# Performance work log

Hardware: AMD Instinct MI355X
Metric: run time of the kernel (lower is better)

Reference implementation:

```python
import jax, jax.numpy as jnp
import numpy as np

# model dims
B, T, D, H, FF, L, V = 2, 1024, 1024, 16, 4096, 2, 32000
DH = D // H          # head dim 64
M = 32               # num attention blocks
BS = T // M          # block size 32
TOPK = 8             # quality-selected blocks per batch element
RATIO = 0.25         # low-pass ratio for spectral quality score
THETA = 10000.0      # rope base
EPS = 1e-6


def setup_inputs() -> dict:
    key = jax.random.key(0)
    ks = jax.random.split(key, 12)
    s = 0.02
    f32 = jnp.float32
    return {
        "input_ids": jax.random.randint(ks[0], (B, T), 0, V),
        "emb": jax.random.normal(ks[1], (V, D), f32) * s,
        "wq": jax.random.normal(ks[2], (L, D, D), f32) * s,
        "wk": jax.random.normal(ks[3], (L, D, D), f32) * s,
        "wv": jax.random.normal(ks[4], (L, D, D), f32) * s,
        "wo": jax.random.normal(ks[5], (L, D, D), f32) * s,
        "w1": jax.random.normal(ks[6], (L, D, FF), f32) * s,
        "w2": jax.random.normal(ks[7], (L, FF, D), f32) * s,
        "w3": jax.random.normal(ks[8], (L, D, FF), f32) * s,
        "attn_norm": jnp.ones((L, D), f32),
        "ffn_norm": jnp.ones((L, D), f32),
        "final_norm": jnp.ones((D,), f32),
        "lm_head": jax.random.normal(ks[9], (D, V), f32) * s,
    }


def _rms(x, w):
    return x * jax.lax.rsqrt(jnp.mean(x * x, axis=-1, keepdims=True) + EPS) * w


def _rope_tables():
    inv = 1.0 / (THETA ** (jnp.arange(0, DH, 2, dtype=jnp.float32) / DH))
    pos = jnp.arange(T, dtype=jnp.float32)
    freqs = pos[:, None] * inv[None, :]            # [T, DH/2]
    emb = jnp.concatenate([freqs, freqs], axis=-1)  # [T, DH]
    return jnp.cos(emb)[None, None], jnp.sin(emb)[None, None]  # [1,1,T,DH]


def _rotate_half(x):
    h = x.shape[-1] // 2
    return jnp.concatenate([-x[..., h:], x[..., :h]], axis=-1)


def _quality_score(h):
    # spectral quality rho(t): low-frequency energy ratio along the sequence axis
    Hf = jnp.fft.rfft(h, axis=1)                   # [B, T//2+1, D] complex
    nf = Hf.shape[1]
    keep = max(1, int(nf * RATIO))
    lp_mask = (jnp.arange(nf) < keep)[None, :, None]
    h_lp = jnp.fft.irfft(jnp.where(lp_mask, Hf, 0.0), n=T, axis=1)
    return jnp.sum(h_lp * h_lp, axis=-1) / (jnp.sum(h * h, axis=-1) + EPS)  # [B,T]


def _forward(input_ids, emb, wq, wk, wv, wo, w1, w2, w3,
             attn_norm, ffn_norm, final_norm, lm_head):
    x = emb[input_ids]                             # [B,T,D]

    # per-token quality (computed once, cached across layers) -> block quality
    rho = _quality_score(x)                        # [B,T]
    blk_quality = rho.reshape(B, M, BS).mean(axis=-1)  # [B,M]

    # quality routing: select top-k blocks per batch element
    _, sel_idx = jax.lax.top_k(blk_quality, TOPK)  # [B,TOPK]
    selected = jnp.zeros((B, M), dtype=bool).at[jnp.arange(B)[:, None], sel_idx].set(True)

    # block-sparse causal mask: causal AND (kv block selected OR same block as query)
    blk_id = jnp.arange(T) // BS                   # [T]
    causal = jnp.tril(jnp.ones((T, T), dtype=bool))
    same_block = blk_id[:, None] == blk_id[None, :]
    allowed_kv = selected[:, blk_id]               # [B,T]
    mask = causal[None] & (allowed_kv[:, None, :] | same_block[None])  # [B,T,T]
    bias = jnp.where(mask, 0.0, -1e9)[:, None]     # [B,1,T,T]

    cos, sin = _rope_tables()
    scale = 1.0 / np.sqrt(DH)

    for l in range(L):
        # attention
        h = _rms(x, attn_norm[l])
        q = (h @ wq[l]).reshape(B, T, H, DH).transpose(0, 2, 1, 3)
        k = (h @ wk[l]).reshape(B, T, H, DH).transpose(0, 2, 1, 3)
        v = (h @ wv[l]).reshape(B, T, H, DH).transpose(0, 2, 1, 3)
        q = q * cos + _rotate_half(q) * sin
        k = k * cos + _rotate_half(k) * sin
        scores = jnp.einsum('bhqd,bhkd->bhqk', q, k) * scale + bias
        attn = jax.nn.softmax(scores, axis=-1)
        o = jnp.einsum('bhqk,bhkd->bhqd', attn, v).transpose(0, 2, 1, 3).reshape(B, T, D)
        x = x + o @ wo[l]
        # swiglu feed-forward
        h = _rms(x, ffn_norm[l])
        x = x + (jax.nn.silu(h @ w1[l]) * (h @ w3[l])) @ w2[l]

    x = _rms(x, final_norm)
    return x @ lm_head                             # [B,T,V]


def reference(input_ids, emb, wq, wk, wv, wo, w1, w2, w3,
              attn_norm, ffn_norm, final_norm, lm_head):
    return _forward(input_ids, emb, wq, wk, wv, wo, w1, w2, w3,
                    attn_norm, ffn_norm, final_norm, lm_head)
```

## Files before the change

kernel.cpp:

```cpp
#include <hip/hip_runtime.h>
#include <hip/hip_bf16.h>

#define Bn 2
#define Tn 1024
#define Dn 1024
#define Hn 16
#define DHn 64
#define FFn 4096
#define Ln 2
#define Vn 32000
#define GM 2048

typedef unsigned short u16;
typedef __attribute__((ext_vector_type(4))) float f4;
typedef __attribute__((ext_vector_type(4))) unsigned short us4;
typedef __attribute__((ext_vector_type(8))) unsigned short us8;
typedef __attribute__((ext_vector_type(8))) short short8;
typedef __attribute__((ext_vector_type(4))) float f32x4;

__device__ __forceinline__ u16 f2b(float x) {
  union { __hip_bfloat16 h; u16 u; } v; v.h = __float2bfloat16(x); return v.u;
}
__device__ __forceinline__ float b2f(u16 u) {
  union { unsigned int i; float f; } v; v.i = ((unsigned int)u) << 16; return v.f;
}
__device__ __forceinline__ float wred64(float v) {
#pragma unroll
  for (int m = 32; m > 0; m >>= 1) v += __shfl_xor(v, m);
  return v;
}
__device__ __forceinline__ void gload_lds16(const void* g, void* l) {
  __builtin_amdgcn_global_load_lds(
      (const __attribute__((address_space(1))) unsigned int*)g,
      (__attribute__((address_space(3))) unsigned int*)l, 16, 0, 0);
}

__global__ void rope_tab_kernel(float* COS, float* SIN) {
  int t = blockIdx.x;
  int j = threadIdx.x;
  float inv = __expf(-(float)(j & 31) * (9.210340371976184f / 32.f));
  float th = (float)t * inv;
  COS[t * 64 + j] = cosf(th);
  SIN[t * 64 + j] = sinf(th);
}

__global__ __launch_bounds__(256) void embed_kernel(const int* ids, const float* emb, float* x) {
  int g = blockIdx.x;
  int id = ids[g];
  const f4* src = (const f4*)(emb + (size_t)id * Dn);
  f4* dst = (f4*)(x + (size_t)g * Dn);
  dst[threadIdx.x] = src[threadIdx.x];
}

__global__ __launch_bounds__(256) void qa_kernel(const float* x, float* Ac, float* Bc) {
  __shared__ float ct[1024], st[1024];
  int blk = blockIdx.x;
  int b = blk >> 7, f = blk & 127;
  for (int t = threadIdx.x; t < 1024; t += 256) {
    float u = (float)((f * t) & 1023) * (6.283185307179586f / 1024.f);
    ct[t] = cosf(u); st[t] = sinf(u);
  }
  __syncthreads();
  int d0 = threadIdx.x * 4;
  f4 a = {0.f,0.f,0.f,0.f}, bb = {0.f,0.f,0.f,0.f};
  const float* xb = x + (size_t)b * Tn * Dn + d0;
  for (int t = 0; t < 1024; ++t) {
    f4 xv = *(const f4*)(xb + (size_t)t * Dn);
    float c = ct[t], s = st[t];
    a += xv * c; bb += xv * s;
  }
  size_t o = ((size_t)b * 128 + f) * Dn + d0;
  *(f4*)(Ac + o) = a; *(f4*)(Bc + o) = bb;
}

__global__ __launch_bounds__(256) void qr_kernel(const float* Ac, const float* Bc,
                                                 const float* x, float* rho) {
  __shared__ float phc[128][4], phs[128][4];
  __shared__ float redN[4], redD[4];
  int blk = blockIdx.x;
  int b = blk >> 8, t0 = (blk & 255) * 4;
  int tid = threadIdx.x;
#pragma unroll
  for (int rep = 0; rep < 2; ++rep) {
    int e = rep * 256 + tid;
    int f = e >> 2, tt = e & 3;
    float u = (float)((f * (t0 + tt)) & 1023) * (6.283185307179586f / 1024.f);
    phc[f][tt] = cosf(u); phs[f][tt] = sinf(u);
  }
  int d0 = tid * 4;
  const float* Ab = Ac + (size_t)b * 128 * Dn + d0;
  const float* Bb = Bc + (size_t)b * 128 * Dn + d0;
  f4 a0 = *(const f4*)Ab;
  float sacc[4][4];
#pragma unroll
  for (int tt = 0; tt < 4; ++tt)
#pragma unroll
    for (int c = 0; c < 4; ++c) sacc[tt][c] = 0.5f * a0[c];
  __syncthreads();
  for (int f = 1; f < 128; ++f) {
    f4 a = *(const f4*)(Ab + (size_t)f * Dn);
    f4 bb = *(const f4*)(Bb + (size_t)f * Dn);
#pragma unroll
    for (int tt = 0; tt < 4; ++tt) {
      float c = phc[f][tt], s = phs[f][tt];
#pragma unroll
      for (int e = 0; e < 4; ++e) sacc[tt][e] += a[e] * c + bb[e] * s;
    }
  }
  int wave = tid >> 6, lane = tid & 63;
  for (int tt = 0; tt < 4; ++tt) {
    f4 xv = *(const f4*)(x + ((size_t)b * Tn + t0 + tt) * Dn + d0);
    float num = 0.f, den = 0.f;
#pragma unroll
    for (int e = 0; e < 4; ++e) {
      float hl = sacc[tt][e] * (2.f / 1024.f);
      num += hl * hl;
      den += xv[e] * xv[e];
    }
    float rn = wred64(num), rd = wred64(den);
    if (lane == 0) { redN[wave] = rn; redD[wave] = rd; }
    __syncthreads();
    if (tid == 0) {
      float n = redN[0] + redN[1] + redN[2] + redN[3];
      float dd = redD[0] + redD[1] + redD[2] + redD[3];
      rho[(size_t)b * Tn + t0 + tt] = n / (dd + 1e-6f);
    }
    __syncthreads();
  }
}

__global__ void topk_kernel(const float* rho, int* sel) {
  __shared__ float bq[32];
  __shared__ int chosen[32];
  int b = blockIdx.x;
  int m = threadIdx.x;
  float s = 0.f;
  for (int j = 0; j < 32; ++j) s += rho[(size_t)b * Tn + m * 32 + j];
  bq[m] = s * (1.f / 32.f); chosen[m] = 0;
  __syncthreads();
  if (m == 0) {
    for (int it = 0; it < 8; ++it) {
      float best = -3e38f; int bi = 0;
      for (int mm = 0; mm < 32; ++mm) if (bq[mm] > best) { best = bq[mm]; bi = mm; }
      chosen[bi] = 1; bq[bi] = -3e38f;
    }
  }
  __syncthreads();
  sel[b * 32 + m] = chosen[m];
}

__global__ __launch_bounds__(256) void transpose_to_bf16(const float* src, u16* dst, int K, int N) {
  __shared__ float tile[32][33];
  int n0 = blockIdx.x * 32, k0 = blockIdx.y * 32;
  int c = threadIdx.x & 31, r4 = threadIdx.x >> 5;
#pragma unroll
  for (int rr = 0; rr < 4; ++rr) {
    int r = r4 * 4 + rr;
    tile[r][c] = src[(size_t)(k0 + r) * N + n0 + c];
  }
  __syncthreads();
#pragma unroll
  for (int rr = 0; rr < 4; ++rr) {
    int r = r4 * 4 + rr;
    dst[(size_t)(n0 + r) * K + k0 + c] = f2b(tile[c][r]);
  }
}

__global__ __launch_bounds__(256) void rmsnorm_kernel(const float* x, const float* w, u16* out) {
  __shared__ float red[4];
  int g = blockIdx.x;
  int tid = threadIdx.x;
  f4 xv = ((const f4*)(x + (size_t)g * Dn))[tid];
  float ss = xv[0]*xv[0] + xv[1]*xv[1] + xv[2]*xv[2] + xv[3]*xv[3];
  ss = wred64(ss);
  if ((tid & 63) == 0) red[tid >> 6] = ss;
  __syncthreads();
  float tot = red[0] + red[1] + red[2] + red[3];
  float r = rsqrtf(tot * (1.f / 1024.f) + 1e-6f);
  f4 wv = ((const f4*)w)[tid];
  us4 o;
#pragma unroll
  for (int e = 0; e < 4; ++e) o[e] = f2b(xv[e] * r * wv[e]);
  *(us4*)(out + (size_t)g * Dn + tid * 4) = o;
}

__global__ __launch_bounds__(256) void gemm_bf16_kernel(
    const u16* __restrict__ A, const u16* __restrict__ Bt,
    void* C, const float* R, int Ni, int Ki, int obf) {
  __shared__ short8 As[1024];
  __shared__ short8 Bs[1024];
  const int tid = threadIdx.x;
  const int wave = tid >> 6, lane = tid & 63;
  const int wr = wave >> 1, wc = wave & 1;
  const int lrow = lane & 15, lkg = lane >> 4;
  const size_t arow0 = (size_t)blockIdx.y * 128;
  const size_t bcol0 = (size_t)blockIdx.x * 128;
  const f32x4 zero4 = {0.f, 0.f, 0.f, 0.f};
  f32x4 acc[4][4];
#pragma unroll
  for (int i = 0; i < 4; ++i)
#pragma unroll
    for (int j = 0; j < 4; ++j) acc[i][j] = zero4;
  const int nK = Ki >> 6;
  for (int kb = 0; kb < nK; ++kb) {
    const size_t k0 = (size_t)kb << 6;
#pragma unroll
    for (int j = 0; j < 4; ++j) {
      const int p = j * 256 + tid;
      const int r = p >> 3, c = p & 7;
      const int cs = c ^ (r & 7);
      gload_lds16(A + (arow0 + r) * Ki + k0 + cs * 8, (char*)As + p * 16);
      gload_lds16(Bt + (bcol0 + r) * Ki + k0 + cs * 8, (char*)Bs + p * 16);
    }
    __syncthreads();
#pragma unroll
    for (int kk = 0; kk < 2; ++kk) {
      short8 af[4], bfr[4];
#pragma unroll
      for (int i = 0; i < 4; ++i) {
        const int ar = wr * 64 + i * 16 + lrow;
        const int akg = kk * 4 + lkg;
        af[i] = *(const short8*)((const char*)As + ar * 128 + ((akg ^ (ar & 7)) << 4));
        const int br = wc * 64 + i * 16 + lrow;
        bfr[i] = *(const short8*)((const char*)Bs + br * 128 + ((akg ^ (br & 7)) << 4));
      }
#pragma unroll
      for (int i = 0; i < 4; ++i)
#pragma unroll
        for (int j = 0; j < 4; ++j)
          acc[i][j] = __builtin_amdgcn_mfma_f32_16x16x32_bf16(af[i], bfr[j], acc[i][j], 0, 0, 0);
    }
    __syncthreads();
  }
  const int crow = (lane >> 4) * 4;
  const int ccol = lane & 15;
#pragma unroll
  for (int i = 0; i < 4; ++i)
#pragma unroll
    for (int j = 0; j < 4; ++j)
#pragma unroll
      for (int rg = 0; rg < 4; ++rg) {
        const size_t grow = arow0 + wr * 64 + i * 16 + crow + rg;
        const size_t gcol = bcol0 + wc * 64 + j * 16 + ccol;
        float v = acc[i][j][rg];
        if (obf) {
          ((u16*)C)[grow * Ni + gcol] = f2b(v);
        } else {
          if (R) v += R[grow * Ni + gcol];
          ((float*)C)[grow * Ni + gcol] = v;
        }
      }
}

__global__ __launch_bounds__(256) void rope_apply_kernel(const float* QKV, const float* COS, const float* SIN,
                                                         float* QRo, float* KRo, float* VRo) {
  int g = blockIdx.x;
  int b = g >> 10, t = g & 1023;
  int j = threadIdx.x * 4;
  int h = j >> 6, jd = j & 63;
  const float* base = QKV + (size_t)g * 3072;
  f4 q = *(const f4*)(base + j);
  f4 k = *(const f4*)(base + 1024 + j);
  f4 v = *(const f4*)(base + 2048 + j);
  int pj = (jd < 32) ? j + 32 : j - 32;
  f4 qp = *(const f4*)(base + pj);
  f4 kp = *(const f4*)(base + 1024 + pj);
  float sgn = (jd < 32) ? -1.f : 1.f;
  f4 cv = *(const f4*)(COS + t * 64 + jd);
  f4 sv = *(const f4*)(SIN + t * 64 + jd);
  f4 qr = q * cv + (qp * sgn) * sv;
  f4 kr = k * cv + (kp * sgn) * sv;
  size_t o = ((size_t)(b * Hn + h) * Tn + t) * 64 + jd;
  *(f4*)(QRo + o) = qr; *(f4*)(KRo + o) = kr; *(f4*)(VRo + o) = v;
}

__global__ __launch_bounds__(256) void attn_kernel(
    const float* __restrict__ QR, const float* __restrict__ KR, const float* __restrict__ VR,
    const int* __restrict__ sel, u16* __restrict__ O) {
  __shared__ float Qs[32][64], Ks[32][64], Vs[32][64], S[32][32];
  const int blk = blockIdx.x;
  const int mq = blk & 31, h = (blk >> 5) & 15, b = blk >> 9;
  const int tid = threadIdx.x;
  const size_t bh = (size_t)(b * Hn + h) * Tn;
  {
    const f4* q4 = (const f4*)(QR + (bh + mq * 32) * 64);
    f4* s4 = (f4*)&Qs[0][0];
    s4[tid] = q4[tid]; s4[tid + 256] = q4[tid + 256];
  }
  const int row = tid >> 3, dg = tid & 7;
  const int dh0 = dg * 8;
  f4 acc0 = {0.f,0.f,0.f,0.f}, acc1 = {0.f,0.f,0.f,0.f};
  float m_i = -3e38f, l_i = 0.f;
  for (int mk = 0; mk <= mq; ++mk) {
    if (!(sel[b * 32 + mk] | (mk == mq))) continue;
    __syncthreads();
    {
      const f4* k4 = (const f4*)(KR + (bh + mk * 32) * 64);
      const f4* v4 = (const f4*)(VR + (bh + mk * 32) * 64);
      ((f4*)Ks)[tid] = k4[tid]; ((f4*)Ks)[tid + 256] = k4[tid + 256];
      ((f4*)Vs)[tid] = v4[tid]; ((f4*)Vs)[tid + 256] = v4[tid + 256];
    }
    __syncthreads();
#pragma unroll
    for (int c = 0; c < 4; ++c) {
      const int idx = tid * 4 + c;
      const int qi = idx >> 5, kj = idx & 31;
      const f4* qv = (const f4*)Qs[qi];
      const f4* kv = (const f4*)Ks[kj];
      f4 sv = {0.f,0.f,0.f,0.f};
#pragma unroll
      for (int d = 0; d < 16; ++d) sv += qv[d] * kv[d];
      float s = (sv[0] + sv[1] + sv[2] + sv[3]) * 0.125f;
      if (mk == mq && kj > qi) s = -3e38f;
      S[qi][kj] = s;
    }
    __syncthreads();
    float mx = m_i;
#pragma unroll
    for (int j2 = 0; j2 < 32; ++j2) mx = fmaxf(mx, S[row][j2]);
    const float resc = __expf(m_i - mx);
    float pv[4]; float psum = 0.f;
#pragma unroll
    for (int c = 0; c < 4; ++c) {
      pv[c] = __expf(S[row][dg * 4 + c] - mx);
      psum += pv[c];
    }
    __syncthreads();
#pragma unroll
    for (int c = 0; c < 4; ++c) S[row][dg * 4 + c] = pv[c];
    psum += __shfl_xor(psum, 1);
    psum += __shfl_xor(psum, 2);
    psum += __shfl_xor(psum, 4);
    l_i = l_i * resc + psum;
    m_i = mx;
    acc0 *= resc; acc1 *= resc;
    __syncthreads();
#pragma unroll
    for (int kj = 0; kj < 32; ++kj) {
      const float p = S[row][kj];
      const f4* vv = (const f4*)&Vs[kj][dh0];
      acc0 += vv[0] * p; acc1 += vv[1] * p;
    }
  }
  const float inv = 1.f / l_i;
  us8 o;
#pragma unroll
  for (int e = 0; e < 4; ++e) { o[e] = f2b(acc0[e] * inv); o[4 + e] = f2b(acc1[e] * inv); }
  const int t = mq * 32 + row;
  *(us8*)(O + (size_t)(b * Tn + t) * Dn + h * 64 + dh0) = o;
}

__global__ __launch_bounds__(256) void silu_mul_b_kernel(const u16* G13b, u16* U) {
  int m = blockIdx.x;
  const u16* g1 = G13b + (size_t)m * 8192;
  const u16* g3 = g1 + 4096;
  int tid = threadIdx.x;
#pragma unroll
  for (int c = 0; c < 2; ++c) {
    int i = tid + 256 * c;
    us8 a = ((const us8*)g1)[i];
    us8 bb = ((const us8*)g3)[i];
    us8 o;
#pragma unroll
    for (int e = 0; e < 8; ++e) {
      float av = b2f(a[e]), bv = b2f(bb[e]);
      float s = av / (1.f + __expf(-av));
      o[e] = f2b(s * bv);
    }
    ((us8*)(U + (size_t)m * 4096))[i] = o;
  }
}

extern "C" void kernel_launch(void* const* d_in, const int* in_sizes, int n_in,
                              void* d_out, int out_size, void* d_ws, size_t ws_size,
                              hipStream_t stream) {
  const int*   ids   = (const int*)d_in[0];
  const float* emb   = (const float*)d_in[1];
  const float* wq    = (const float*)d_in[2];
  const float* wk    = (const float*)d_in[3];
  const float* wv    = (const float*)d_in[4];
  const float* wo    = (const float*)d_in[5];
  const float* w1    = (const float*)d_in[6];
  const float* w2    = (const float*)d_in[7];
  const float* w3    = (const float*)d_in[8];
  const float* anrm  = (const float*)d_in[9];
  const float* fnrm  = (const float*)d_in[10];
  const float* finrm = (const float*)d_in[11];
  const float* lmw   = (const float*)d_in[12];
  float* out = (float*)d_out;

  char* ws = (char*)d_ws;
  size_t off = 0;
  auto alloc = [&](size_t sz) { void* p = ws + off; off += (sz + 255) & ~(size_t)255; return p; };
  const size_t MB = 1024ull * 1024ull;

  float* X    = (float*)alloc((size_t)GM * Dn * 4);
  u16*   Hb   = (u16*)alloc((size_t)GM * Dn * 2);
  float* COS  = (float*)alloc((size_t)Tn * 64 * 4);
  float* SIN  = (float*)alloc((size_t)Tn * 64 * 4);
  int*   SEL  = (int*)alloc(256);
  u16*   QKVl = (u16*)alloc((size_t)3072 * 1024 * 2);
  u16*   WOl  = (u16*)alloc((size_t)1024 * 1024 * 2);
  u16*   W13l = (u16*)alloc((size_t)8192 * 1024 * 2);
  u16*   W2l  = (u16*)alloc((size_t)1024 * 4096 * 2);
  char*  SCR  = (char*)alloc(66 * MB);

  if (off > ws_size) return;

  float* Ac  = (float*)SCR;
  float* Bc  = (float*)(SCR + 1 * MB);
  float* RHO = (float*)(SCR + 2 * MB);
  float* QKVf = (float*)SCR;
  float* QRb  = (float*)(SCR + 24 * MB);
  float* KRb  = (float*)(SCR + 32 * MB);
  float* VRb  = (float*)(SCR + 40 * MB);
  u16*   Ob   = (u16*)(SCR + 48 * MB);
  u16*   G13b = (u16*)SCR;
  u16*   Ub   = (u16*)(SCR + 32 * MB);
  u16*   LMT  = (u16*)SCR;

  rope_tab_kernel<<<Tn, 64, 0, stream>>>(COS, SIN);
  embed_kernel<<<GM, 256, 0, stream>>>(ids, emb, X);
  qa_kernel<<<Bn * 128, 256, 0, stream>>>(X, Ac, Bc);
  qr_kernel<<<Bn * 256, 256, 0, stream>>>(Ac, Bc, X, RHO);
  topk_kernel<<<Bn, 32, 0, stream>>>(RHO, SEL);

  for (int l = 0; l < Ln; ++l) {
    const size_t dd = (size_t)1024 * 1024;
    const size_t df = (size_t)1024 * 4096;
    transpose_to_bf16<<<dim3(32, 32), 256, 0, stream>>>(wq + l * dd, QKVl, 1024, 1024);
    transpose_to_bf16<<<dim3(32, 32), 256, 0, stream>>>(wk + l * dd, QKVl + dd, 1024, 1024);
    transpose_to_bf16<<<dim3(32, 32), 256, 0, stream>>>(wv + l * dd, QKVl + 2 * dd, 1024, 1024);
    transpose_to_bf16<<<dim3(32, 32), 256, 0, stream>>>(wo + l * dd, WOl, 1024, 1024);
    transpose_to_bf16<<<dim3(128, 32), 256, 0, stream>>>(w1 + l * df, W13l, 1024, 4096);
    transpose_to_bf16<<<dim3(128, 32), 256, 0, stream>>>(w3 + l * df, W13l + df, 1024, 4096);
    transpose_to_bf16<<<dim3(32, 128), 256, 0, stream>>>(w2 + l * df, W2l, 4096, 1024);

    rmsnorm_kernel<<<GM, 256, 0, stream>>>(X, anrm + l * Dn, Hb);
    gemm_bf16_kernel<<<dim3(24, 16), 256, 0, stream>>>(Hb, QKVl, QKVf, nullptr, 3072, 1024, 0);
    rope_apply_kernel<<<GM, 256, 0, stream>>>(QKVf, COS, SIN, QRb, KRb, VRb);
    attn_kernel<<<Bn * Hn * 32, 256, 0, stream>>>(QRb, KRb, VRb, SEL, Ob);
    gemm_bf16_kernel<<<dim3(8, 16), 256, 0, stream>>>(Ob, WOl, X, X, 1024, 1024, 0);
    rmsnorm_kernel<<<GM, 256, 0, stream>>>(X, fnrm + l * Dn, Hb);
    gemm_bf16_kernel<<<dim3(64, 16), 256, 0, stream>>>(Hb, W13l, G13b, nullptr, 8192, 1024, 1);
    silu_mul_b_kernel<<<GM, 256, 0, stream>>>(G13b, Ub);
    gemm_bf16_kernel<<<dim3(8, 16), 256, 0, stream>>>(Ub, W2l, X, X, 1024, 4096, 0);
  }

  transpose_to_bf16<<<dim3(1000, 32), 256, 0, stream>>>(lmw, LMT, 1024, Vn);
  rmsnorm_kernel<<<GM, 256, 0, stream>>>(X, finrm, Hb);
  gemm_bf16_kernel<<<dim3(250, 16), 256, 0, stream>>>(Hb, LMT, out, nullptr, Vn, 1024, 0);
}
```

Measured before the change: 1.596 ms.

## Fuse RoPE and SwiGLU into GEMM epilogues, interleave W1/W3, faster transpose

Folds the RoPE application into the QKV GEMM epilogue and SiLU*gate into the W1/W3 GEMM epilogue. It does this by interleaving W1 and W3 rows in 16-row groups so each tile holds matching gate and up columns. This drops the fp32 QKV and bf16 G13 intermediate round trips and two kernel launches. It also replaces the 32x32 transpose with a 64x64 tile that uses vector loads and stores. A 1D grid remap spreads adjacent blocks across XCD-strided tiles for cache locality, at the cost of more complex epilogue indexing and scattered non-coalesced stores.

```diff
diff --git a/kernel.cpp b/kernel.cpp
--- a/kernel.cpp
+++ b/kernel.cpp
@@ -149,21 +149,28 @@
   sel[b * 32 + m] = chosen[m];
 }
 
-__global__ __launch_bounds__(256) void transpose_to_bf16(const float* src, u16* dst, int K, int N) {
-  __shared__ float tile[32][33];
-  int n0 = blockIdx.x * 32, k0 = blockIdx.y * 32;
-  int c = threadIdx.x & 31, r4 = threadIdx.x >> 5;
-#pragma unroll
-  for (int rr = 0; rr < 4; ++rr) {
-    int r = r4 * 4 + rr;
-    tile[r][c] = src[(size_t)(k0 + r) * N + n0 + c];
-  }
-  __syncthreads();
-#pragma unroll
-  for (int rr = 0; rr < 4; ++rr) {
-    int r = r4 * 4 + rr;
-    dst[(size_t)(n0 + r) * K + k0 + c] = f2b(tile[c][r]);
-  }
+__global__ __launch_bounds__(256) void transpose64(const float* __restrict__ src, u16* __restrict__ dst,
+                                                   int K, int N, int rowmul, int rowadd) {
+  __shared__ u16 tile[64][72];
+  const int n0 = blockIdx.x * 64, k0 = blockIdx.y * 64;
+  const int tid = threadIdx.x;
+  const int r = tid >> 2;
+  const int c0 = (tid & 3) * 16;
+  const float* s = src + (size_t)(k0 + r) * N + n0 + c0;
+#pragma unroll
+  for (int q = 0; q < 4; ++q) {
+    f4 v = *(const f4*)(s + q * 4);
+#pragma unroll
+    for (int e = 0; e < 4; ++e) tile[c0 + q * 4 + e][r] = f2b(v[e]);
+  }
+  __syncthreads();
+  const int n = n0 + r;
+  const size_t drow = (size_t)((n >> 4) * rowmul + rowadd + (n & 15));
+  us8* d = (us8*)(dst + drow * K + k0 + c0);
+  us8 o0, o1;
+#pragma unroll
+  for (int e = 0; e < 8; ++e) { o0[e] = tile[r][c0 + e]; o1[e] = tile[r][c0 + 8 + e]; }
+  d[0] = o0; d[1] = o1;
 }
 
 __global__ __launch_bounds__(256) void rmsnorm_kernel(const float* x, const float* w, u16* out) {
@@ -184,17 +191,24 @@
   *(us4*)(out + (size_t)g * Dn + tid * 4) = o;
 }
 
-__global__ __launch_bounds__(256) void gemm_bf16_kernel(
+template<int EPI>
+__global__ __launch_bounds__(256) void gemm_bf16(
     const u16* __restrict__ A, const u16* __restrict__ Bt,
-    void* C, const float* R, int Ni, int Ki, int obf) {
+    float* C, const float* R, u16* U,
+    float* QRo, float* KRo, float* VRo, const float* __restrict__ COS, const float* __restrict__ SIN,
+    int Ni, int Ki, int cf) {
   __shared__ short8 As[1024];
   __shared__ short8 Bs[1024];
   const int tid = threadIdx.x;
   const int wave = tid >> 6, lane = tid & 63;
   const int wr = wave >> 1, wc = wave & 1;
   const int lrow = lane & 15, lkg = lane >> 4;
-  const size_t arow0 = (size_t)blockIdx.y * 128;
-  const size_t bcol0 = (size_t)blockIdx.x * 128;
+  const int lg = (blockIdx.x & 7) * ((int)gridDim.x >> 3) + ((int)blockIdx.x >> 3);
+  int bx, by;
+  if (cf) { const int nbx = Ni >> 7; bx = lg % nbx; by = lg / nbx; }
+  else    { by = lg & 15; bx = lg >> 4; }
+  const size_t arow0 = (size_t)by * 128;
+  const size_t bcol0 = (size_t)bx * 128;
   const f32x4 zero4 = {0.f, 0.f, 0.f, 0.f};
   f32x4 acc[4][4];
 #pragma unroll
@@ -234,44 +248,60 @@
   }
   const int crow = (lane >> 4) * 4;
   const int ccol = lane & 15;
-#pragma unroll
-  for (int i = 0; i < 4; ++i)
-#pragma unroll
-    for (int j = 0; j < 4; ++j)
+  if (EPI == 0) {
+#pragma unroll
+    for (int i = 0; i < 4; ++i)
+#pragma unroll
+      for (int j = 0; j < 4; ++j)
+#pragma unroll
+        for (int rg = 0; rg < 4; ++rg) {
+          const size_t grow = arow0 + wr * 64 + i * 16 + crow + rg;
+          const size_t gcol = bcol0 + wc * 64 + j * 16 + ccol;
+          float v = acc[i][j][rg];
+          if (R) v += R[grow * Ni + gcol];
+          C[grow * Ni + gcol] = v;
+        }
+  } else if (EPI == 2) {
+    const int sec = (int)(bcol0 >> 10);
+    const int hh = (((int)bcol0 & 1023) >> 6) + wc;
+    float* dstQK = (sec == 0) ? QRo : KRo;
+#pragma unroll
+    for (int i = 0; i < 4; ++i)
+#pragma unroll
+      for (int rg = 0; rg < 4; ++rg) {
+        const int t = (int)arow0 + wr * 64 + i * 16 + crow + rg;
+        const int bb = t >> 10, tt = t & 1023;
+        const size_t obase = ((size_t)(bb * Hn + hh) * Tn + tt) * 64;
+#pragma unroll
+        for (int j = 0; j < 4; ++j) {
+          const int jd = j * 16 + ccol;
+          const float v = acc[i][j][rg];
+          if (sec < 2) {
+            const float p = acc[i][j ^ 2][rg];
+            const float cs = COS[tt * 64 + jd], sn = SIN[tt * 64 + jd];
+            dstQK[obase + jd] = v * cs + ((j < 2) ? -p : p) * sn;
+          } else {
+            VRo[obase + jd] = v;
+          }
+        }
+      }
+  } else if (EPI == 3) {
+#pragma unroll
+    for (int i = 0; i < 4; ++i)
 #pragma unroll
       for (int rg = 0; rg < 4; ++rg) {
         const size_t grow = arow0 + wr * 64 + i * 16 + crow + rg;
-        const size_t gcol = bcol0 + wc * 64 + j * 16 + ccol;
-        float v = acc[i][j][rg];
-        if (obf) {
-          ((u16*)C)[grow * Ni + gcol] = f2b(v);
-        } else {
-          if (R) v += R[grow * Ni + gcol];
-          ((float*)C)[grow * Ni + gcol] = v;
+#pragma unroll
+        for (int jp = 0; jp < 2; ++jp) {
+          const int j = jp * 2;
+          const float a = acc[i][j][rg];
+          const float g3 = acc[i][j + 1][rg];
+          const float s = (a / (1.f + __expf(-a))) * g3;
+          const int f = ((((int)bcol0 + wc * 64 + j * 16) >> 5) << 4) + ccol;
+          U[grow * 4096 + f] = f2b(s);
         }
       }
-}
-
-__global__ __launch_bounds__(256) void rope_apply_kernel(const float* QKV, const float* COS, const float* SIN,
-                                                         float* QRo, float* KRo, float* VRo) {
-  int g = blockIdx.x;
-  int b = g >> 10, t = g & 1023;
-  int j = threadIdx.x * 4;
-  int h = j >> 6, jd = j & 63;
-  const float* base = QKV + (size_t)g * 3072;
-  f4 q = *(const f4*)(base + j);
-  f4 k = *(const f4*)(base + 1024 + j);
-  f4 v = *(const f4*)(base + 2048 + j);
-  int pj = (jd < 32) ? j + 32 : j - 32;
-  f4 qp = *(const f4*)(base + pj);
-  f4 kp = *(const f4*)(base + 1024 + pj);
-  float sgn = (jd < 32) ? -1.f : 1.f;
-  f4 cv = *(const f4*)(COS + t * 64 + jd);
-  f4 sv = *(const f4*)(SIN + t * 64 + jd);
-  f4 qr = q * cv + (qp * sgn) * sv;
-  f4 kr = k * cv + (kp * sgn) * sv;
-  size_t o = ((size_t)(b * Hn + h) * Tn + t) * 64 + jd;
-  *(f4*)(QRo + o) = qr; *(f4*)(KRo + o) = kr; *(f4*)(VRo + o) = v;
+  }
 }
 
 __global__ __launch_bounds__(256) void attn_kernel(
@@ -348,27 +378,6 @@
   for (int e = 0; e < 4; ++e) { o[e] = f2b(acc0[e] * inv); o[4 + e] = f2b(acc1[e] * inv); }
   const int t = mq * 32 + row;
   *(us8*)(O + (size_t)(b * Tn + t) * Dn + h * 64 + dh0) = o;
-}
-
-__global__ __launch_bounds__(256) void silu_mul_b_kernel(const u16* G13b, u16* U) {
-  int m = blockIdx.x;
-  const u16* g1 = G13b + (size_t)m * 8192;
-  const u16* g3 = g1 + 4096;
-  int tid = threadIdx.x;
-#pragma unroll
-  for (int c = 0; c < 2; ++c) {
-    int i = tid + 256 * c;
-    us8 a = ((const us8*)g1)[i];
-    us8 bb = ((const us8*)g3)[i];
-    us8 o;
-#pragma unroll
-    for (int e = 0; e < 8; ++e) {
-      float av = b2f(a[e]), bv = b2f(bb[e]);
-      float s = av / (1.f + __expf(-av));
-      o[e] = f2b(s * bv);
-    }
-    ((us8*)(U + (size_t)m * 4096))[i] = o;
-  }
 }
 
 extern "C" void kernel_launch(void* const* d_in, const int* in_sizes, int n_in,
@@ -410,13 +419,11 @@
   float* Ac  = (float*)SCR;
   float* Bc  = (float*)(SCR + 1 * MB);
   float* RHO = (float*)(SCR + 2 * MB);
-  float* QKVf = (float*)SCR;
   float* QRb  = (float*)(SCR + 24 * MB);
   float* KRb  = (float*)(SCR + 32 * MB);
   float* VRb  = (float*)(SCR + 40 * MB);
   u16*   Ob   = (u16*)(SCR + 48 * MB);
-  u16*   G13b = (u16*)SCR;
-  u16*   Ub   = (u16*)(SCR + 32 * MB);
+  u16*   Ub   = (u16*)(SCR + 0 * MB);
   u16*   LMT  = (u16*)SCR;
 
   rope_tab_kernel<<<Tn, 64, 0, stream>>>(COS, SIN);
@@ -428,26 +435,29 @@
   for (int l = 0; l < Ln; ++l) {
     const size_t dd = (size_t)1024 * 1024;
     const size_t df = (size_t)1024 * 4096;
-    transpose_to_bf16<<<dim3(32, 32), 256, 0, stream>>>(wq + l * dd, QKVl, 1024, 1024);
-    transpose_to_bf16<<<dim3(32, 32), 256, 0, stream>>>(wk + l * dd, QKVl + dd, 1024, 1024);
-    transpose_to_bf16<<<dim3(32, 32), 256, 0, stream>>>(wv + l * dd, QKVl + 2 * dd, 1024, 1024);
-    transpose_to_bf16<<<dim3(32, 32), 256, 0, stream>>>(wo + l * dd, WOl, 1024, 1024);
-    transpose_to_bf16<<<dim3(128, 32), 256, 0, stream>>>(w1 + l * df, W13l, 1024, 4096);
-    transpose_to_bf16<<<dim3(128, 32), 256, 0, stream>>>(w3 + l * df, W13l + df, 1024, 4096);
-    transpose_to_bf16<<<dim3(32, 128), 256, 0, stream>>>(w2 + l * df, W2l, 4096, 1024);
+    transpose64<<<dim3(16, 16), 256, 0, stream>>>(wq + l * dd, QKVl, 1024, 1024, 16, 0);
+    transpose64<<<dim3(16, 16), 256, 0, stream>>>(wk + l * dd, QKVl + dd, 1024, 1024, 16, 0);
+    transpose64<<<dim3(16, 16), 256, 0, stream>>>(wv + l * dd, QKVl + 2 * dd, 1024, 1024, 16, 0);
+    transpose64<<<dim3(16, 16), 256, 0, stream>>>(wo + l * dd, WOl, 1024, 1024, 16, 0);
+    transpose64<<<dim3(64, 16), 256, 0, stream>>>(w1 + l * df, W13l, 1024, 4096, 32, 0);
+    transpose64<<<dim3(64, 16), 256, 0, stream>>>(w3 + l * df, W13l, 1024, 4096, 32, 16);
+    transpose64<<<dim3(16, 64), 256, 0, stream>>>(w2 + l * df, W2l, 4096, 1024, 16, 0);
 
     rmsnorm_kernel<<<GM, 256, 0, stream>>>(X, anrm + l * Dn, Hb);
-    gemm_bf16_kernel<<<dim3(24, 16), 256, 0, stream>>>(Hb, QKVl, QKVf, nullptr, 3072, 1024, 0);
-    rope_apply_kernel<<<GM, 256, 0, stream>>>(QKVf, COS, SIN, QRb, KRb, VRb);
+    gemm_bf16<2><<<384, 256, 0, stream>>>(Hb, QKVl, nullptr, nullptr, nullptr,
+                                          QRb, KRb, VRb, COS, SIN, 3072, 1024, 0);
     attn_kernel<<<Bn * Hn * 32, 256, 0, stream>>>(QRb, KRb, VRb, SEL, Ob);
-    gemm_bf16_kernel<<<dim3(8, 16), 256, 0, stream>>>(Ob, WOl, X, X, 1024, 1024, 0);
+    gemm_bf16<0><<<128, 256, 0, stream>>>(Ob, WOl, X, X, nullptr,
+                                          nullptr, nullptr, nullptr, nullptr, nullptr, 1024, 1024, 1);
     rmsnorm_kernel<<<GM, 256, 0, stream>>>(X, fnrm + l * Dn, Hb);
-    gemm_bf16_kernel<<<dim3(64, 16), 256, 0, stream>>>(Hb, W13l, G13b, nullptr, 8192, 1024, 1);
-    silu_mul_b_kernel<<<GM, 256, 0, stream>>>(G13b, Ub);
-    gemm_bf16_kernel<<<dim3(8, 16), 256, 0, stream>>>(Ub, W2l, X, X, 1024, 4096, 0);
-  }
-
-  transpose_to_bf16<<<dim3(1000, 32), 256, 0, stream>>>(lmw, LMT, 1024, Vn);
+    gemm_bf16<3><<<1024, 256, 0, stream>>>(Hb, W13l, nullptr, nullptr, Ub,
+                                           nullptr, nullptr, nullptr, nullptr, nullptr, 8192, 1024, 0);
+    gemm_bf16<0><<<128, 256, 0, stream>>>(Ub, W2l, X, X, nullptr,
+                                          nullptr, nullptr, nullptr, nullptr, nullptr, 1024, 4096, 1);
+  }
+
+  transpose64<<<dim3(500, 16), 256, 0, stream>>>(lmw, LMT, 1024, Vn, 16, 0);
   rmsnorm_kernel<<<GM, 256, 0, stream>>>(X, finrm, Hb);
-  gemm_bf16_kernel<<<dim3(250, 16), 256, 0, stream>>>(Hb, LMT, out, nullptr, Vn, 1024, 0);
-}
+  gemm_bf16<0><<<4000, 256, 0, stream>>>(Hb, LMT, out, nullptr, nullptr,
+                                         nullptr, nullptr, nullptr, nullptr, nullptr, Vn, 1024, 0);
+}
```

Result: no change. 1.582 ms (-0.9%).
